# Performance work log

Hardware: AMD Instinct MI355X
Metric: run time of the kernel (lower is better)

The kernel has to match this reference:

```python
import jax, jax.numpy as jnp
import numpy as np

B, D, L, H, W, T = 256, 512, 32, 14, 14, 8


def _lin(x, w, b=None):
    y = x @ w.T
    return y if b is None else y + b


def _conv1x1(x, w, b):  # x: [B,C,H,W], w: [O,C], b: [O]
    return jnp.einsum('oc,bchw->bohw', w, x) + b[None, :, None, None]


def setup_inputs() -> dict:
    key = jax.random.key(0)
    ks = jax.random.split(key, 24)
    s = 0.02
    inp = {
        'c': jax.random.normal(ks[0], (B, D), jnp.float32),
        'm': jax.random.normal(ks[1], (B, D), jnp.float32),
        'k': jax.random.normal(ks[2], (B, D, H, W), jnp.float32),
        'q': jax.random.normal(ks[3], (B, D), jnp.float32),
        'cw': jax.random.normal(ks[4], (B, L, D), jnp.float32),
        'mask': jax.random.randint(ks[5], (B, L), 0, 2, jnp.int32),
        'cs': jax.random.normal(ks[6], (T, B, D), jnp.float32),
        'ms': jax.random.normal(ks[7], (T, B, D), jnp.float32),
        # ControlUnit params
        'Wcq': jax.random.normal(ks[8], (D, 2 * D), jnp.float32) * s,
        'bcq': jnp.zeros((D,), jnp.float32),
        'Wca': jax.random.normal(ks[9], (1, D), jnp.float32) * s,
        'bca': jnp.zeros((1,), jnp.float32),
        # ReadUnit params
        'Wm_r': jax.random.normal(ks[10], (D, D), jnp.float32) * s,
        'bm_r': jnp.zeros((D,), jnp.float32),
        'Wk': jax.random.normal(ks[11], (D, D), jnp.float32) * s,
        'bk': jnp.zeros((D,), jnp.float32),
        'WI': jax.random.normal(ks[12], (D, 2 * D), jnp.float32) * s,
        'bI': jnp.zeros((D,), jnp.float32),
        'Wra': jax.random.normal(ks[13], (D, D), jnp.float32) * s,
        'bra': jnp.zeros((D,), jnp.float32),
        # WriteUnit params
        'Wm_w': jax.random.normal(ks[14], (D, 2 * D), jnp.float32) * s,
        'bm_w': jnp.zeros((D,), jnp.float32),
        'Wsa': jax.random.normal(ks[15], (1, D), jnp.float32) * s,
        'bsa': jnp.zeros((1,), jnp.float32),
        'Wm2': jax.random.normal(ks[16], (D, D), jnp.float32) * s,
        'bm2': jnp.zeros((D,), jnp.float32),
        'Wc': jax.random.normal(ks[17], (1, D), jnp.float32) * s,
        'bc': jnp.ones((1,), jnp.float32),  # linear_c.bias.data.fill_(1)
        'Ws': jax.random.normal(ks[18], (D, D), jnp.float32) * s,
    }
    return inp


def reference(c, m, k, q, cw, mask, cs, ms,
              Wcq, bcq, Wca, bca,
              Wm_r, bm_r, Wk, bk, WI, bI, Wra, bra,
              Wm_w, bm_w, Wsa, bsa, Wm2, bm2, Wc, bc, Ws):
    # ---- ControlUnit ----
    cq = _lin(jnp.concatenate([c, q], axis=1), Wcq, bcq)          # [B,D]
    ca = _lin(cq[:, None, :] * cw, Wca, bca)                      # [B,L,1]
    ca = jnp.where(mask[:, :, None] > 0, ca, -jnp.inf)            # mask padding
    cv = jax.nn.softmax(ca, axis=1)                               # [B,L,1]
    c_new = jnp.sum(cv * cw, axis=1)                              # [B,D]

    # ---- ReadUnit ----
    mI = _lin(m, Wm_r, bm_r)                                      # [B,D]
    I = mI[:, :, None, None] * _conv1x1(k, Wk, bk)                # [B,D,H,W]
    I_ = _conv1x1(jnp.concatenate([I, k], axis=1), WI, bI)        # [B,D,H,W]
    ra = _conv1x1(I_ * c_new[:, :, None, None], Wra, bra)         # [B,D,H,W]
    rv = jax.nn.softmax(ra, axis=1)                               # Softmax2d = over channels
    r = jnp.sum(rv * k, axis=(-1, -2))                            # [B,D]

    # ---- WriteUnit ----
    m_prev = _lin(jnp.concatenate([r, m], axis=1), Wm_w, bm_w)    # [B,D]
    m_ = _lin(m_prev, Wm2, bm2)                                   # [B,D]
    gate = jax.nn.sigmoid(_lin(c_new, Wc, bc))                    # [B,1]
    sa = jax.nn.softmax(_lin(cs * gate[None, :, :], Wsa, bsa), axis=0)  # [T,B,1]
    m_sa = jnp.sum(sa * ms, axis=0)                               # [B,D]
    m_ = m_ + m_sa @ Ws.T
    m_new = gate * m + (1.0 - gate) * m_                          # [B,D]

    return (c_new, m_new, cv, rv)
```

## Files before the change

### kernel.cpp

```cpp
#include <hip/hip_runtime.h>
#include <hip/hip_bf16.h>

#define BB 256
#define DD 512
#define LL 32
#define HWN 196
#define TT 8
#define STEPB 12544

typedef __hip_bfloat16 bf16;
typedef __attribute__((ext_vector_type(8))) short short8;
typedef __attribute__((ext_vector_type(4))) float f32x4;

__device__ __forceinline__ float b2f(bf16 x) { return __bfloat162float(x); }
__device__ __forceinline__ unsigned short f2bu(float x) {
    bf16 h = __float2bfloat16(x);
    return *(unsigned short*)&h;
}
#define NEG_INF (-__builtin_huge_valf())

__device__ __forceinline__ void gload_lds16(const void* g, void* l) {
    __builtin_amdgcn_global_load_lds(
        (const __attribute__((address_space(1))) void*)g,
        (__attribute__((address_space(3))) void*)l, 16, 0, 0);
}
__device__ __forceinline__ void gload_lds4(const void* g, void* l) {
    __builtin_amdgcn_global_load_lds(
        (const __attribute__((address_space(1))) void*)g,
        (__attribute__((address_space(3))) void*)l, 4, 0, 0);
}

__global__ __launch_bounds__(256) void cvt_w_kernel(
    const float* __restrict__ src, unsigned short* __restrict__ dst, int n4)
{
    int i = blockIdx.x*256 + threadIdx.x;
    if (i < n4) {
        float4 f = ((const float4*)src)[i];
        ushort4 u;
        u.x = f2bu(f.x); u.y = f2bu(f.y); u.z = f2bu(f.z); u.w = f2bu(f.w);
        ((ushort4*)dst)[i] = u;
    }
}

__global__ __launch_bounds__(256) void pack_x_kernel(
    const float* __restrict__ X, char* __restrict__ Xp)
{
    int b = blockIdx.x, s = blockIdx.y;
    char* chunk = Xp + ((size_t)(b*16 + s))*STEPB;
    for (int i = threadIdx.x; i < 4*HWN; i += 256) {
        int n = i >> 2, kqp = i & 3;
        const float* base = X + ((size_t)b*DD + s*32 + kqp*8)*HWN + n;
        uint v[4];
        #pragma unroll
        for (int h = 0; h < 4; ++h) {
            float f0 = base[(size_t)(2*h+0)*HWN], f1 = base[(size_t)(2*h+1)*HWN];
            v[h] = (uint)f2bu(f0) | ((uint)f2bu(f1) << 16);
        }
        *(uint4*)(chunk + n*64 + kqp*16) = make_uint4(v[0], v[1], v[2], v[3]);
    }
}

__global__ __launch_bounds__(256) void small_gemm_kernel(
    const float* __restrict__ A1, int K1,
    const float* __restrict__ A2, int K2,
    const float* __restrict__ Wt, const float* __restrict__ bias,
    float* __restrict__ outf, int Dout)
{
    __shared__ float xs[1024];
    int b = blockIdx.x, tid = threadIdx.x;
    int K = K1 + K2;
    for (int i = tid; i < K; i += 256) {
        xs[i] = (i < K1) ? A1[(size_t)b*K1 + i] : A2[(size_t)b*K2 + (i - K1)];
    }
    __syncthreads();
    for (int d = tid; d < Dout; d += 256) {
        const float4* wrow = (const float4*)(Wt + (size_t)d * K);
        float acc = 0.f;
        for (int j = 0; j < K/4; ++j) {
            float4 w = wrow[j];
            acc += w.x*xs[j*4] + w.y*xs[j*4+1] + w.z*xs[j*4+2] + w.w*xs[j*4+3];
        }
        if (bias) acc += bias[d];
        outf[(size_t)b*Dout + d] = acc;
    }
}

__global__ __launch_bounds__(256) void control_kernel(
    const float* __restrict__ cq, const float* __restrict__ cw,
    const float* __restrict__ Wca, const float* __restrict__ bca,
    const int* __restrict__ mask,
    float* __restrict__ cnew_f, float* __restrict__ cv_out, float* __restrict__ cnew_out)
{
    __shared__ float u[DD];
    __shared__ float cas[LL];
    __shared__ float cvs[LL];
    int b = blockIdx.x, tid = threadIdx.x;
    for (int d = tid; d < DD; d += 256) u[d] = cq[(size_t)b*DD + d] * Wca[d];
    __syncthreads();
    int wave = tid >> 6, lane = tid & 63;
    float bca0 = bca[0];
    for (int lw = 0; lw < 8; ++lw) {
        int l = wave*8 + lw;
        const float4* w4 = (const float4*)(cw + ((size_t)(b*LL + l))*DD + lane*8);
        float4 wa = w4[0], wb = w4[1];
        const float* uu = &u[lane*8];
        float p = wa.x*uu[0] + wa.y*uu[1] + wa.z*uu[2] + wa.w*uu[3]
                + wb.x*uu[4] + wb.y*uu[5] + wb.z*uu[6] + wb.w*uu[7];
        for (int off = 32; off > 0; off >>= 1) p += __shfl_down(p, off);
        if (lane == 0) {
            float v = p + bca0;
            if (mask[b*LL + l] <= 0) v = NEG_INF;
            cas[l] = v;
        }
    }
    __syncthreads();
    if (tid < LL) {
        float mx = NEG_INF;
        for (int j = 0; j < LL; ++j) mx = fmaxf(mx, cas[j]);
        float s = 0.f;
        for (int j = 0; j < LL; ++j) s += __expf(cas[j] - mx);
        float cv = __expf(cas[tid] - mx) / s;
        cvs[tid] = cv;
        cv_out[b*LL + tid] = cv;
    }
    __syncthreads();
    for (int d = tid; d < DD; d += 256) {
        float acc = 0.f;
        for (int l = 0; l < LL; ++l) acc += cvs[l] * cw[((size_t)(b*LL + l))*DD + d];
        cnew_f[(size_t)b*DD + d] = acc;
        cnew_out[(size_t)b*DD + d] = acc;
    }
}

__global__ __launch_bounds__(512) void conv_mfma_kernel(
    const char* __restrict__ X1p, int ns1,
    const char* __restrict__ X2p, int ns2,
    const unsigned short* __restrict__ Wb, int C,
    const float* __restrict__ bias, const float* __restrict__ oscale,
    void* __restrict__ Yout, int packed_out)
{
    __shared__ __align__(16) char Xs[4][12800];
    int b = blockIdx.x, ot = blockIdx.y;
    int tid = threadIdx.x;
    int wave = tid >> 6, lane = tid & 63;
    int wm = wave >> 1, wn = wave & 1;
    int obase = ot*128 + wm*32;
    int n0 = wn*112;
    int ntn = wn ? 6 : 7;
    int ln = lane & 15, lq = lane >> 4;
    int nsteps = ns1 + ns2;

    auto STAGE = [&](int s) {
        const char* chunk = (s < ns1) ? X1p + ((size_t)b*ns1 + s)*STEPB
                                      : X2p + ((size_t)b*ns2 + (s - ns1))*STEPB;
        char* lb = Xs[s & 3];
        gload_lds16(chunk + wave*1024 + lane*16, lb + wave*1024);
        if (wave < 5)       gload_lds16(chunk + (wave+8)*1024 + lane*16, lb + (wave+8)*1024);
        else if (wave == 7) gload_lds4 (chunk + 12288 + lane*4, lb + 12288);
    };
    auto ALOAD = [&](int s, short8& a0, short8& a1) {
        a0 = *(const short8*)(Wb + (size_t)(obase + ln)*C + s*32 + lq*8);
        a1 = *(const short8*)(Wb + (size_t)(obase + 16 + ln)*C + s*32 + lq*8);
    };

    f32x4 acc[2][7];
    #pragma unroll
    for (int mt = 0; mt < 2; ++mt)
        #pragma unroll
        for (int nt = 0; nt < 7; ++nt) acc[mt][nt] = (f32x4){0.f, 0.f, 0.f, 0.f};

    short8 a0c, a1c, a0n, a1n;

    STAGE(0);
    STAGE(1);
    __builtin_amdgcn_sched_barrier(0);
    ALOAD(0, a0c, a1c);
    __builtin_amdgcn_sched_barrier(0);
    STAGE(2);

    auto BODY = [&](int s, bool doA, bool doX) {
        __builtin_amdgcn_s_barrier();
        if (doA) ALOAD(s + 1, a0n, a1n);
        __builtin_amdgcn_sched_barrier(0);
        if (doX) STAGE(s + 3);
        __builtin_amdgcn_sched_barrier(0);
        const char* curb = Xs[s & 3];
        #pragma unroll
        for (int nt = 0; nt < 7; ++nt) {
            if (nt < ntn) {
                int n = n0 + nt*16 + ln;
                union { uint4 u; short8 s8; } bb;
                bb.u = *(const uint4*)(curb + n*64 + lq*16);
                acc[0][nt] = __builtin_amdgcn_mfma_f32_16x16x32_bf16(a0c, bb.s8, acc[0][nt], 0, 0, 0);
                acc[1][nt] = __builtin_amdgcn_mfma_f32_16x16x32_bf16(a1c, bb.s8, acc[1][nt], 0, 0, 0);
            }
        }
        a0c = a0n; a1c = a1n;
    };

    for (int s = 0; s <= nsteps - 4; ++s) {
        asm volatile("s_waitcnt vmcnt(2)" ::: "memory");
        __builtin_amdgcn_sched_barrier(0);
        BODY(s, true, true);
    }
    {
        asm volatile("s_waitcnt vmcnt(2)" ::: "memory");
        __builtin_amdgcn_sched_barrier(0);
        BODY(nsteps - 3, true, false);
    }
    {
        asm volatile("s_waitcnt vmcnt(0)" ::: "memory");
        __builtin_amdgcn_sched_barrier(0);
        BODY(nsteps - 2, true, false);
    }
    {
        asm volatile("s_waitcnt vmcnt(0)" ::: "memory");
        __builtin_amdgcn_sched_barrier(0);
        BODY(nsteps - 1, false, false);
    }

    if (packed_out) {
        uint2* Yp = (uint2*)Yout;
        #pragma unroll
        for (int mt = 0; mt < 2; ++mt) {
            int o4 = obase + mt*16 + lq*4;
            int st = o4 >> 5, kqo = (o4 & 31) >> 2;
            uint2* chunk = Yp + (size_t)(b*16 + st)*1568;
            float bo[4], os[4];
            #pragma unroll
            for (int rr = 0; rr < 4; ++rr) {
                bo[rr] = bias[o4 + rr];
                os[rr] = oscale ? oscale[(size_t)b*DD + o4 + rr] : 1.f;
            }
            #pragma unroll
            for (int nt = 0; nt < 7; ++nt) {
                int hw = n0 + nt*16 + ln;
                if (nt < ntn && hw < HWN) {
                    unsigned short v[4];
                    #pragma unroll
                    for (int rr = 0; rr < 4; ++rr)
                        v[rr] = f2bu((acc[mt][nt][rr] + bo[rr]) * os[rr]);
                    chunk[hw*8 + kqo] =
                        make_uint2((uint)v[0] | ((uint)v[1] << 16),
                                   (uint)v[2] | ((uint)v[3] << 16));
                }
            }
        }
    } else {
        unsigned short* Y = (unsigned short*)Yout;
        #pragma unroll
        for (int mt = 0; mt < 2; ++mt) {
            #pragma unroll
            for (int rr = 0; rr < 4; ++rr) {
                int o = obase + mt*16 + lq*4 + rr;
                float bo = bias[o];
                float os = oscale ? oscale[(size_t)b*DD + o] : 1.f;
                #pragma unroll
                for (int nt = 0; nt < 7; ++nt) {
                    int hw = n0 + nt*16 + ln;
                    if (nt < ntn && hw < HWN) {
                        float v = (acc[mt][nt][rr] + bo) * os;
                        Y[((size_t)b*DD + o)*HWN + hw] = f2bu(v);
                    }
                }
            }
        }
    }
}

__global__ __launch_bounds__(512) void softmax_r_kernel(
    const bf16* __restrict__ ra, const float* __restrict__ kin,
    float* __restrict__ rv, float* __restrict__ r)
{
    __shared__ float pm[2][HWN], ps[2][HWN];
    __shared__ float mxs[HWN], sis[HWN];
    int b = blockIdx.x, tid = threadIdx.x;
    int half = tid >> 8, hw = tid & 255;
    if (hw < HWN) {
        float m = NEG_INF, s = 0.f;
        const bf16* base = ra + ((size_t)b*DD + half*256)*HWN + hw;
        for (int c = 0; c < 256; ++c) {
            float x = b2f(base[(size_t)c*HWN]);
            float nm = fmaxf(m, x);
            s = s*__expf(m - nm) + __expf(x - nm);
            m = nm;
        }
        pm[half][hw] = m; ps[half][hw] = s;
    }
    __syncthreads();
    if (tid < HWN) {
        float m0 = pm[0][tid], m1 = pm[1][tid];
        float m = fmaxf(m0, m1);
        float s = ps[0][tid]*__expf(m0 - m) + ps[1][tid]*__expf(m1 - m);
        mxs[tid] = m; sis[tid] = 1.f/s;
    }
    __syncthreads();
    int wave = tid >> 6, lane = tid & 63;
    for (int ci = 0; ci < 64; ++ci) {
        int c = wave*64 + ci;
        float psum = 0.f;
        #pragma unroll
        for (int g = 0; g < 4; ++g) {
            int hw2 = lane + 64*g;
            if (hw2 < HWN) {
                size_t idx = ((size_t)b*DD + c)*HWN + hw2;
                float e = __expf(b2f(ra[idx]) - mxs[hw2]) * sis[hw2];
                rv[idx] = e;
                psum += e * kin[idx];
            }
        }
        for (int off = 32; off > 0; off >>= 1) psum += __shfl_down(psum, off);
        if (lane == 0) r[(size_t)b*DD + c] = psum;
    }
}

__global__ __launch_bounds__(256) void samsa_kernel(
    const float* __restrict__ cs, const float* __restrict__ ms,
    const float* __restrict__ Wsa, const float* __restrict__ bsa,
    const float* __restrict__ cnew, const float* __restrict__ Wc, const float* __restrict__ bc,
    float* __restrict__ gate_out, float* __restrict__ msa)
{
    __shared__ float lg[TT];
    __shared__ float sas[TT];
    __shared__ float xw[DD];
    __shared__ float gsh;
    int b = blockIdx.x, tid = threadIdx.x;
    int wave = tid >> 6, lane = tid & 63;
    for (int d = tid; d < DD; d += 256) xw[d] = Wsa[d];
    __syncthreads();
    for (int tw = 0; tw < 2; ++tw) {
        int t = wave + 4*tw;
        const float4* c4 = (const float4*)(cs + ((size_t)t*BB + b)*DD + lane*8);
        float4 ca = c4[0], cb = c4[1];
        const float* ww = &xw[lane*8];
        float p = ca.x*ww[0] + ca.y*ww[1] + ca.z*ww[2] + ca.w*ww[3]
                + cb.x*ww[4] + cb.y*ww[5] + cb.z*ww[6] + cb.w*ww[7];
        for (int off = 32; off > 0; off >>= 1) p += __shfl_down(p, off);
        if (lane == 0) lg[t] = p;
    }
    if (wave == 0) {
        const float4* w4 = (const float4*)(Wc + lane*8);
        const float* x = &cnew[(size_t)b*DD + lane*8];
        float4 wa = w4[0], wb = w4[1];
        float p = wa.x*x[0] + wa.y*x[1] + wa.z*x[2] + wa.w*x[3]
                + wb.x*x[4] + wb.y*x[5] + wb.z*x[6] + wb.w*x[7];
        for (int off = 32; off > 0; off >>= 1) p += __shfl_down(p, off);
        if (lane == 0) {
            float g = 1.f / (1.f + __expf(-(p + bc[0])));
            gsh = g; gate_out[b] = g;
        }
    }
    __syncthreads();
    if (tid < TT) {
        float g = gsh, b0 = bsa[0];
        float mx = NEG_INF;
        for (int j = 0; j < TT; ++j) mx = fmaxf(mx, g*lg[j] + b0);
        float s = 0.f;
        for (int j = 0; j < TT; ++j) s += __expf(g*lg[j] + b0 - mx);
        sas[tid] = __expf(g*lg[tid] + b0 - mx) / s;
    }
    __syncthreads();
    for (int d = tid; d < DD; d += 256) {
        float acc = 0.f;
        for (int t = 0; t < TT; ++t) acc += sas[t] * ms[((size_t)t*BB + b)*DD + d];
        msa[(size_t)b*DD + d] = acc;
    }
}

__global__ __launch_bounds__(256) void write_final_kernel(
    const float* __restrict__ msa, const float* __restrict__ Ws,
    const float* __restrict__ m, const float* __restrict__ gate,
    const float* __restrict__ mund, float* __restrict__ mnew)
{
    __shared__ float xs[DD];
    int b = blockIdx.x, tid = threadIdx.x;
    for (int i = tid; i < DD; i += 256) xs[i] = msa[(size_t)b*DD + i];
    __syncthreads();
    float g = gate[b];
    for (int d = tid; d < DD; d += 256) {
        const float4* wrow = (const float4*)(Ws + (size_t)d * DD);
        float acc = 0.f;
        for (int j = 0; j < DD/4; ++j) {
            float4 w = wrow[j];
            acc += w.x*xs[j*4] + w.y*xs[j*4+1] + w.z*xs[j*4+2] + w.w*xs[j*4+3];
        }
        size_t idx = (size_t)b*DD + d;
        mnew[idx] = g * m[idx] + (1.f - g) * (mund[idx] + acc);
    }
}

extern "C" void kernel_launch(void* const* d_in, const int* in_sizes, int n_in,
                              void* d_out, int out_size, void* d_ws, size_t ws_size,
                              hipStream_t stream)
{
    (void)in_sizes; (void)n_in; (void)out_size; (void)ws_size;
    const float* c    = (const float*)d_in[0];
    const float* m    = (const float*)d_in[1];
    const float* k    = (const float*)d_in[2];
    const float* q    = (const float*)d_in[3];
    const float* cw   = (const float*)d_in[4];
    const int*   mask = (const int*)  d_in[5];
    const float* cs   = (const float*)d_in[6];
    const float* ms   = (const float*)d_in[7];
    const float* Wcq  = (const float*)d_in[8];
    const float* bcq  = (const float*)d_in[9];
    const float* Wca  = (const float*)d_in[10];
    const float* bca  = (const float*)d_in[11];
    const float* Wm_r = (const float*)d_in[12];
    const float* bm_r = (const float*)d_in[13];
    const float* Wk   = (const float*)d_in[14];
    const float* bk   = (const float*)d_in[15];
    const float* WI   = (const float*)d_in[16];
    const float* bI   = (const float*)d_in[17];
    const float* Wra  = (const float*)d_in[18];
    const float* bra  = (const float*)d_in[19];
    const float* Wm_w = (const float*)d_in[20];
    const float* bm_w = (const float*)d_in[21];
    const float* Wsa  = (const float*)d_in[22];
    const float* bsa  = (const float*)d_in[23];
    const float* Wm2  = (const float*)d_in[24];
    const float* bm2  = (const float*)d_in[25];
    const float* Wc   = (const float*)d_in[26];
    const float* bc   = (const float*)d_in[27];
    const float* Ws   = (const float*)d_in[28];

    float* out_cnew = (float*)d_out;
    float* out_mnew = out_cnew + BB*DD;
    float* out_cv   = out_mnew + BB*DD;
    float* out_rv   = out_cv + BB*LL;

    char* Ip  = (char*)out_rv;
    char* I2p = (char*)out_rv + 51380224;

    char* w = (char*)d_ws;
    float* s0      = (float*)(w + 0);
    float* s1      = (float*)(w + 524288);
    float* s2      = (float*)(w + 1048576);
    float* s3      = (float*)(w + 1572864);
    unsigned short* Wkb  = (unsigned short*)(w + 2097152);
    unsigned short* WIb  = (unsigned short*)(w + 2621440);
    unsigned short* Wrab = (unsigned short*)(w + 3670016);
    char* kp_ra = (char*)(w + 4194304);
    float* gate_w  = (float*)(w + 55574528);

    float* cq_w   = s0;
    float* r_w    = s0;
    float* cnew_w = s1;
    float* mI_w   = s2;
    float* mund_w = s2;
    float* mprev_w= s3;
    float* msa_w  = s3;
    unsigned short* ra_w = (unsigned short*)kp_ra;

    cvt_w_kernel<<<256, 256, 0, stream>>>(Wk,  Wkb,  65536);
    cvt_w_kernel<<<512, 256, 0, stream>>>(WI,  WIb,  131072);
    cvt_w_kernel<<<256, 256, 0, stream>>>(Wra, Wrab, 65536);

    pack_x_kernel<<<dim3(BB, 16), 256, 0, stream>>>(k, kp_ra);

    small_gemm_kernel<<<BB, 256, 0, stream>>>(c, DD, q, DD, Wcq, bcq, cq_w, DD);
    small_gemm_kernel<<<BB, 256, 0, stream>>>(m, DD, nullptr, 0, Wm_r, bm_r, mI_w, DD);
    control_kernel<<<BB, 256, 0, stream>>>(cq_w, cw, Wca, bca, mask, cnew_w, out_cv, out_cnew);

    conv_mfma_kernel<<<dim3(BB, 4), 512, 0, stream>>>(kp_ra, 16, nullptr, 0,  Wkb,  DD,   bk,  mI_w,   Ip,   1);
    conv_mfma_kernel<<<dim3(BB, 4), 512, 0, stream>>>(Ip,    16, kp_ra,  16,  WIb,  2*DD, bI,  cnew_w, I2p,  1);
    conv_mfma_kernel<<<dim3(BB, 4), 512, 0, stream>>>(I2p,   16, nullptr, 0,  Wrab, DD,   bra, nullptr, ra_w, 0);
    softmax_r_kernel<<<BB, 512, 0, stream>>>((const bf16*)ra_w, k, out_rv, r_w);

    small_gemm_kernel<<<BB, 256, 0, stream>>>(r_w, DD, m, DD, Wm_w, bm_w, mprev_w, DD);
    small_gemm_kernel<<<BB, 256, 0, stream>>>(mprev_w, DD, nullptr, 0, Wm2, bm2, mund_w, DD);
    samsa_kernel<<<BB, 256, 0, stream>>>(cs, ms, Wsa, bsa, cnew_w, Wc, bc, gate_w, msa_w);
    write_final_kernel<<<BB, 256, 0, stream>>>(msa_w, Ws, m, gate_w, mund_w, out_mnew);
}
```

Baseline: 783.1 us.

## Retile conv MFMA waves, split softmax across blocks, widen small GEMM grids

The conv MFMA kernel gives each wave a 64x48/64 tile instead of 32x112, so each B fragment loaded from LDS feeds four MFMAs instead of two. It also raises launch_bounds occupancy and grows the LDS buffers to cover the padded tiles. The channel softmax is split into a partial max/sum kernel and a normalize kernel over two HW halves, which combine r with atomicAdd and give more blocks. The small GEMV kernels get a second grid dimension over output rows, and the three weight-conversion launches become one. The risks are extra register pressure, reads of uninitialized LDS padding (masked at store), atomics in r, and workspace areas that now overlap with other buffers.

Measured after the change: 950.2 us. 21.3% more time.

```diff
diff --git a/kernel.cpp b/kernel.cpp
--- a/kernel.cpp
+++ b/kernel.cpp
@@ -17,6 +17,10 @@
     bf16 h = __float2bfloat16(x);
     return *(unsigned short*)&h;
 }
+__device__ __forceinline__ float bu2f(unsigned short u) {
+    bf16 h = *(bf16*)&u;
+    return __bfloat162float(h);
+}
 #define NEG_INF (-__builtin_huge_valf())
 
 __device__ __forceinline__ void gload_lds16(const void* g, void* l) {
@@ -30,16 +34,20 @@
         (__attribute__((address_space(3))) void*)l, 4, 0, 0);
 }
 
-__global__ __launch_bounds__(256) void cvt_w_kernel(
-    const float* __restrict__ src, unsigned short* __restrict__ dst, int n4)
-{
-    int i = blockIdx.x*256 + threadIdx.x;
-    if (i < n4) {
-        float4 f = ((const float4*)src)[i];
-        ushort4 u;
-        u.x = f2bu(f.x); u.y = f2bu(f.y); u.z = f2bu(f.z); u.w = f2bu(f.w);
-        ((ushort4*)dst)[i] = u;
-    }
+__global__ __launch_bounds__(256) void cvt3_kernel(
+    const float* __restrict__ s0, unsigned short* __restrict__ d0,
+    const float* __restrict__ s1, unsigned short* __restrict__ d1,
+    const float* __restrict__ s2, unsigned short* __restrict__ d2)
+{
+    int blk = blockIdx.x, tid = threadIdx.x;
+    const float* s; unsigned short* d; int i;
+    if (blk < 256)      { s = s0; d = d0; i = blk*256 + tid; }
+    else if (blk < 768) { s = s1; d = d1; i = (blk-256)*256 + tid; }
+    else                { s = s2; d = d2; i = (blk-768)*256 + tid; }
+    float4 f = ((const float4*)s)[i];
+    ushort4 u;
+    u.x = f2bu(f.x); u.y = f2bu(f.y); u.z = f2bu(f.z); u.w = f2bu(f.w);
+    ((ushort4*)d)[i] = u;
 }
 
 __global__ __launch_bounds__(256) void pack_x_kernel(
@@ -73,16 +81,15 @@
         xs[i] = (i < K1) ? A1[(size_t)b*K1 + i] : A2[(size_t)b*K2 + (i - K1)];
     }
     __syncthreads();
-    for (int d = tid; d < Dout; d += 256) {
-        const float4* wrow = (const float4*)(Wt + (size_t)d * K);
-        float acc = 0.f;
-        for (int j = 0; j < K/4; ++j) {
-            float4 w = wrow[j];
-            acc += w.x*xs[j*4] + w.y*xs[j*4+1] + w.z*xs[j*4+2] + w.w*xs[j*4+3];
-        }
-        if (bias) acc += bias[d];
-        outf[(size_t)b*Dout + d] = acc;
-    }
+    int d = blockIdx.y*256 + tid;
+    const float4* wrow = (const float4*)(Wt + (size_t)d * K);
+    float acc = 0.f;
+    for (int j = 0; j < K/4; ++j) {
+        float4 w = wrow[j];
+        acc += w.x*xs[j*4] + w.y*xs[j*4+1] + w.z*xs[j*4+2] + w.w*xs[j*4+3];
+    }
+    if (bias) acc += bias[d];
+    outf[(size_t)b*Dout + d] = acc;
 }
 
 __global__ __launch_bounds__(256) void control_kernel(
@@ -132,21 +139,21 @@
     }
 }
 
-__global__ __launch_bounds__(512) void conv_mfma_kernel(
+__global__ __launch_bounds__(512, 4) void conv_mfma_kernel(
     const char* __restrict__ X1p, int ns1,
     const char* __restrict__ X2p, int ns2,
     const unsigned short* __restrict__ Wb, int C,
     const float* __restrict__ bias, const float* __restrict__ oscale,
     void* __restrict__ Yout, int packed_out)
 {
-    __shared__ __align__(16) char Xs[4][12800];
+    __shared__ __align__(16) char Xs[4][13312];
     int b = blockIdx.x, ot = blockIdx.y;
     int tid = threadIdx.x;
     int wave = tid >> 6, lane = tid & 63;
-    int wm = wave >> 1, wn = wave & 1;
-    int obase = ot*128 + wm*32;
-    int n0 = wn*112;
-    int ntn = wn ? 6 : 7;
+    int wm = wave >> 2, wn = wave & 3;
+    int obase = ot*128 + wm*64;
+    int t0 = wn*3;
+    int ntn = (wn == 3) ? 4 : 3;
     int ln = lane & 15, lq = lane >> 4;
     int nsteps = ns1 + ns2;
 
@@ -158,44 +165,47 @@
         if (wave < 5)       gload_lds16(chunk + (wave+8)*1024 + lane*16, lb + (wave+8)*1024);
         else if (wave == 7) gload_lds4 (chunk + 12288 + lane*4, lb + 12288);
     };
-    auto ALOAD = [&](int s, short8& a0, short8& a1) {
-        a0 = *(const short8*)(Wb + (size_t)(obase + ln)*C + s*32 + lq*8);
-        a1 = *(const short8*)(Wb + (size_t)(obase + 16 + ln)*C + s*32 + lq*8);
+    auto ALOAD = [&](int s, short8* a) {
+        #pragma unroll
+        for (int mt = 0; mt < 4; ++mt)
+            a[mt] = *(const short8*)(Wb + (size_t)(obase + mt*16 + ln)*C + s*32 + lq*8);
     };
 
-    f32x4 acc[2][7];
+    f32x4 acc[4][4];
     #pragma unroll
-    for (int mt = 0; mt < 2; ++mt)
-        #pragma unroll
-        for (int nt = 0; nt < 7; ++nt) acc[mt][nt] = (f32x4){0.f, 0.f, 0.f, 0.f};
-
-    short8 a0c, a1c, a0n, a1n;
+    for (int mt = 0; mt < 4; ++mt)
+        #pragma unroll
+        for (int nt = 0; nt < 4; ++nt) acc[mt][nt] = (f32x4){0.f, 0.f, 0.f, 0.f};
+
+    short8 a_cur[4], a_nxt[4];
 
     STAGE(0);
     STAGE(1);
     __builtin_amdgcn_sched_barrier(0);
-    ALOAD(0, a0c, a1c);
+    ALOAD(0, a_cur);
     __builtin_amdgcn_sched_barrier(0);
     STAGE(2);
 
     auto BODY = [&](int s, bool doA, bool doX) {
         __builtin_amdgcn_s_barrier();
-        if (doA) ALOAD(s + 1, a0n, a1n);
+        if (doA) ALOAD(s + 1, a_nxt);
         __builtin_amdgcn_sched_barrier(0);
         if (doX) STAGE(s + 3);
         __builtin_amdgcn_sched_barrier(0);
         const char* curb = Xs[s & 3];
         #pragma unroll
-        for (int nt = 0; nt < 7; ++nt) {
+        for (int nt = 0; nt < 4; ++nt) {
             if (nt < ntn) {
-                int n = n0 + nt*16 + ln;
+                int n = (t0 + nt)*16 + ln;
                 union { uint4 u; short8 s8; } bb;
                 bb.u = *(const uint4*)(curb + n*64 + lq*16);
-                acc[0][nt] = __builtin_amdgcn_mfma_f32_16x16x32_bf16(a0c, bb.s8, acc[0][nt], 0, 0, 0);
-                acc[1][nt] = __builtin_amdgcn_mfma_f32_16x16x32_bf16(a1c, bb.s8, acc[1][nt], 0, 0, 0);
+                #pragma unroll
+                for (int mt = 0; mt < 4; ++mt)
+                    acc[mt][nt] = __builtin_amdgcn_mfma_f32_16x16x32_bf16(a_cur[mt], bb.s8, acc[mt][nt], 0, 0, 0);
             }
         }
-        a0c = a0n; a1c = a1n;
+        #pragma unroll
+        for (int mt = 0; mt < 4; ++mt) a_cur[mt] = a_nxt[mt];
     };
 
     for (int s = 0; s <= nsteps - 4; ++s) {
@@ -222,7 +232,7 @@
     if (packed_out) {
         uint2* Yp = (uint2*)Yout;
         #pragma unroll
-        for (int mt = 0; mt < 2; ++mt) {
+        for (int mt = 0; mt < 4; ++mt) {
             int o4 = obase + mt*16 + lq*4;
             int st = o4 >> 5, kqo = (o4 & 31) >> 2;
             uint2* chunk = Yp + (size_t)(b*16 + st)*1568;
@@ -233,8 +243,8 @@
                 os[rr] = oscale ? oscale[(size_t)b*DD + o4 + rr] : 1.f;
             }
             #pragma unroll
-            for (int nt = 0; nt < 7; ++nt) {
-                int hw = n0 + nt*16 + ln;
+            for (int nt = 0; nt < 4; ++nt) {
+                int hw = (t0 + nt)*16 + ln;
                 if (nt < ntn && hw < HWN) {
                     unsigned short v[4];
                     #pragma unroll
@@ -249,15 +259,15 @@
     } else {
         unsigned short* Y = (unsigned short*)Yout;
         #pragma unroll
-        for (int mt = 0; mt < 2; ++mt) {
+        for (int mt = 0; mt < 4; ++mt) {
             #pragma unroll
             for (int rr = 0; rr < 4; ++rr) {
                 int o = obase + mt*16 + lq*4 + rr;
                 float bo = bias[o];
                 float os = oscale ? oscale[(size_t)b*DD + o] : 1.f;
                 #pragma unroll
-                for (int nt = 0; nt < 7; ++nt) {
-                    int hw = n0 + nt*16 + ln;
+                for (int nt = 0; nt < 4; ++nt) {
+                    int hw = (t0 + nt)*16 + ln;
                     if (nt < ntn && hw < HWN) {
                         float v = (acc[mt][nt][rr] + bo) * os;
                         Y[((size_t)b*DD + o)*HWN + hw] = f2bu(v);
@@ -268,49 +278,72 @@
     }
 }
 
-__global__ __launch_bounds__(512) void softmax_r_kernel(
-    const bf16* __restrict__ ra, const float* __restrict__ kin,
-    float* __restrict__ rv, float* __restrict__ r)
-{
-    __shared__ float pm[2][HWN], ps[2][HWN];
-    __shared__ float mxs[HWN], sis[HWN];
-    int b = blockIdx.x, tid = threadIdx.x;
+__global__ __launch_bounds__(512) void softmax_part_kernel(
+    const bf16* __restrict__ ra,
+    unsigned short* __restrict__ pm_part, float* __restrict__ ps_part,
+    float* __restrict__ r_zero)
+{
+    int b = blockIdx.x, y = blockIdx.y, tid = threadIdx.x;
+    if (y == 0) r_zero[(size_t)b*DD + tid] = 0.f;
     int half = tid >> 8, hw = tid & 255;
     if (hw < HWN) {
+        int sl = y*2 + half;
+        const bf16* base = ra + ((size_t)b*DD + sl*64)*HWN + hw;
         float m = NEG_INF, s = 0.f;
-        const bf16* base = ra + ((size_t)b*DD + half*256)*HWN + hw;
-        for (int c = 0; c < 256; ++c) {
+        for (int c = 0; c < 64; ++c) {
             float x = b2f(base[(size_t)c*HWN]);
             float nm = fmaxf(m, x);
             s = s*__expf(m - nm) + __expf(x - nm);
             m = nm;
         }
-        pm[half][hw] = m; ps[half][hw] = s;
-    }
-    __syncthreads();
-    if (tid < HWN) {
-        float m0 = pm[0][tid], m1 = pm[1][tid];
-        float m = fmaxf(m0, m1);
-        float s = ps[0][tid]*__expf(m0 - m) + ps[1][tid]*__expf(m1 - m);
-        mxs[tid] = m; sis[tid] = 1.f/s;
+        unsigned short pmu = f2bu(m);
+        float pmf = bu2f(pmu);
+        s *= __expf(m - pmf);
+        size_t idx = ((size_t)sl*BB + b)*HWN + hw;
+        pm_part[idx] = pmu;
+        ps_part[idx] = s;
+    }
+}
+
+__global__ __launch_bounds__(512) void softmax_rv_kernel(
+    const bf16* __restrict__ ra, const float* __restrict__ kin,
+    const unsigned short* __restrict__ pm_part, const float* __restrict__ ps_part,
+    float* __restrict__ rv, float* __restrict__ r)
+{
+    __shared__ float mxs[98], sis[98];
+    int b = blockIdx.x, h = blockIdx.y, tid = threadIdx.x;
+    int hwb = h*98;
+    if (tid < 98) {
+        int hw = hwb + tid;
+        float pmv[8], mx = NEG_INF;
+        #pragma unroll
+        for (int i = 0; i < 8; ++i) {
+            pmv[i] = bu2f(pm_part[((size_t)i*BB + b)*HWN + hw]);
+            mx = fmaxf(mx, pmv[i]);
+        }
+        float s = 0.f;
+        #pragma unroll
+        for (int i = 0; i < 8; ++i)
+            s += ps_part[((size_t)i*BB + b)*HWN + hw] * __expf(pmv[i] - mx);
+        mxs[tid] = mx; sis[tid] = 1.f/s;
     }
     __syncthreads();
     int wave = tid >> 6, lane = tid & 63;
     for (int ci = 0; ci < 64; ++ci) {
         int c = wave*64 + ci;
+        size_t rowbase = ((size_t)b*DD + c)*HWN + hwb;
         float psum = 0.f;
         #pragma unroll
-        for (int g = 0; g < 4; ++g) {
-            int hw2 = lane + 64*g;
-            if (hw2 < HWN) {
-                size_t idx = ((size_t)b*DD + c)*HWN + hw2;
-                float e = __expf(b2f(ra[idx]) - mxs[hw2]) * sis[hw2];
-                rv[idx] = e;
-                psum += e * kin[idx];
+        for (int g = 0; g < 2; ++g) {
+            int j = g*64 + lane;
+            if (j < 98) {
+                float e = __expf(b2f(ra[rowbase + j]) - mxs[j]) * sis[j];
+                rv[rowbase + j] = e;
+                psum += e * kin[rowbase + j];
             }
         }
         for (int off = 32; off > 0; off >>= 1) psum += __shfl_down(psum, off);
-        if (lane == 0) r[(size_t)b*DD + c] = psum;
+        if (lane == 0) atomicAdd(&r[(size_t)b*DD + c], psum);
     }
 }
 
@@ -377,16 +410,15 @@
     for (int i = tid; i < DD; i += 256) xs[i] = msa[(size_t)b*DD + i];
     __syncthreads();
     float g = gate[b];
-    for (int d = tid; d < DD; d += 256) {
-        const float4* wrow = (const float4*)(Ws + (size_t)d * DD);
-        float acc = 0.f;
-        for (int j = 0; j < DD/4; ++j) {
-            float4 w = wrow[j];
-            acc += w.x*xs[j*4] + w.y*xs[j*4+1] + w.z*xs[j*4+2] + w.w*xs[j*4+3];
-        }
-        size_t idx = (size_t)b*DD + d;
-        mnew[idx] = g * m[idx] + (1.f - g) * (mund[idx] + acc);
-    }
+    int d = blockIdx.y*256 + tid;
+    const float4* wrow = (const float4*)(Ws + (size_t)d * DD);
+    float acc = 0.f;
+    for (int j = 0; j < DD/4; ++j) {
+        float4 w = wrow[j];
+        acc += w.x*xs[j*4] + w.y*xs[j*4+1] + w.z*xs[j*4+2] + w.w*xs[j*4+3];
+    }
+    size_t idx = (size_t)b*DD + d;
+    mnew[idx] = g * m[idx] + (1.f - g) * (mund[idx] + acc);
 }
 
 extern "C" void kernel_launch(void* const* d_in, const int* in_sizes, int n_in,
@@ -435,8 +467,8 @@
     char* w = (char*)d_ws;
     float* s0      = (float*)(w + 0);
     float* s1      = (float*)(w + 524288);
-    float* s2      = (float*)(w + 1048576);
-    float* s3      = (float*)(w + 1572864);
+    unsigned short* pm_part = (unsigned short*)(w + 1048576);
+    float* ps_part = (float*)(w + 2097152);
     unsigned short* Wkb  = (unsigned short*)(w + 2097152);
     unsigned short* WIb  = (unsigned short*)(w + 2621440);
     unsigned short* Wrab = (unsigned short*)(w + 3670016);
@@ -446,29 +478,29 @@
     float* cq_w   = s0;
     float* r_w    = s0;
     float* cnew_w = s1;
-    float* mI_w   = s2;
-    float* mund_w = s2;
-    float* mprev_w= s3;
-    float* msa_w  = s3;
+    float* mI_w   = (float*)(w + 1048576);
+    float* mund_w = (float*)(w + 1048576);
+    float* mprev_w= (float*)(w + 1572864);
+    float* msa_w  = (float*)(w + 1572864);
     unsigned short* ra_w = (unsigned short*)kp_ra;
 
-    cvt_w_kernel<<<256, 256, 0, stream>>>(Wk,  Wkb,  65536);
-    cvt_w_kernel<<<512, 256, 0, stream>>>(WI,  WIb,  131072);
-    cvt_w_kernel<<<256, 256, 0, stream>>>(Wra, Wrab, 65536);
+    cvt3_kernel<<<1024, 256, 0, stream>>>(Wk, Wkb, WI, WIb, Wra, Wrab);
 
     pack_x_kernel<<<dim3(BB, 16), 256, 0, stream>>>(k, kp_ra);
 
-    small_gemm_kernel<<<BB, 256, 0, stream>>>(c, DD, q, DD, Wcq, bcq, cq_w, DD);
-    small_gemm_kernel<<<BB, 256, 0, stream>>>(m, DD, nullptr, 0, Wm_r, bm_r, mI_w, DD);
+    small_gemm_kernel<<<dim3(BB,2), 256, 0, stream>>>(c, DD, q, DD, Wcq, bcq, cq_w, DD);
+    small_gemm_kernel<<<dim3(BB,2), 256, 0, stream>>>(m, DD, nullptr, 0, Wm_r, bm_r, mI_w, DD);
     control_kernel<<<BB, 256, 0, stream>>>(cq_w, cw, Wca, bca, mask, cnew_w, out_cv, out_cnew);
 
     conv_mfma_kernel<<<dim3(BB, 4), 512, 0, stream>>>(kp_ra, 16, nullptr, 0,  Wkb,  DD,   bk,  mI_w,   Ip,   1);
     conv_mfma_kernel<<<dim3(BB, 4), 512, 0, stream>>>(Ip,    16, kp_ra,  16,  WIb,  2*DD, bI,  cnew_w, I2p,  1);
     conv_mfma_kernel<<<dim3(BB, 4), 512, 0, stream>>>(I2p,   16, nullptr, 0,  Wrab, DD,   bra, nullptr, ra_w, 0);
-    softmax_r_kernel<<<BB, 512, 0, stream>>>((const bf16*)ra_w, k, out_rv, r_w);
-
-    small_gemm_kernel<<<BB, 256, 0, stream>>>(r_w, DD, m, DD, Wm_w, bm_w, mprev_w, DD);
-    small_gemm_kernel<<<BB, 256, 0, stream>>>(mprev_w, DD, nullptr, 0, Wm2, bm2, mund_w, DD);
+
+    softmax_part_kernel<<<dim3(BB, 4), 512, 0, stream>>>((const bf16*)ra_w, pm_part, ps_part, r_w);
+    softmax_rv_kernel<<<dim3(BB, 2), 512, 0, stream>>>((const bf16*)ra_w, k, pm_part, ps_part, out_rv, r_w);
+
+    small_gemm_kernel<<<dim3(BB,2), 256, 0, stream>>>(r_w, DD, m, DD, Wm_w, bm_w, mprev_w, DD);
+    small_gemm_kernel<<<dim3(BB,2), 256, 0, stream>>>(mprev_w, DD, nullptr, 0, Wm2, bm2, mund_w, DD);
     samsa_kernel<<<BB, 256, 0, stream>>>(cs, ms, Wsa, bsa, cnew_w, Wc, bc, gate_w, msa_w);
-    write_final_kernel<<<BB, 256, 0, stream>>>(msa_w, Ws, m, gate_w, mund_w, out_mnew);
-}
+    write_final_kernel<<<dim3(BB,2), 256, 0, stream>>>(msa_w, Ws, m, gate_w, mund_w, out_mnew);
+}
```
